# Performance work log

Hardware: AMD Instinct MI355X
Metric: run time of the kernel (lower is better)

Reference implementation:

```python
import jax, jax.numpy as jnp
import numpy as np

N_NODES = 50000
N_EDGES = 600000
IN_DIM = 128
OUT_DIM = 128
NEG_SLOPE = 0.2
LN_EPS = 1e-5


def setup_inputs() -> dict:
    key = jax.random.key(0)
    ks = jax.random.split(key, 8)
    x = jax.random.normal(ks[0], (N_NODES, IN_DIM), dtype=jnp.float32)
    edge_index = jax.random.randint(ks[1], (2, N_EDGES), 0, N_NODES, dtype=jnp.int64)
    glorot = float(np.sqrt(6.0 / (IN_DIM + OUT_DIM)))
    W_l = jax.random.uniform(ks[2], (IN_DIM, OUT_DIM), jnp.float32, -glorot, glorot)
    W_r = jax.random.uniform(ks[3], (IN_DIM, OUT_DIM), jnp.float32, -glorot, glorot)
    att = jax.random.uniform(ks[4], (OUT_DIM,), jnp.float32, -glorot, glorot)
    bias = jnp.zeros((OUT_DIM,), jnp.float32)
    ln_gamma = jnp.ones((OUT_DIM,), jnp.float32)
    ln_beta = jnp.zeros((OUT_DIM,), jnp.float32)
    return {"x": x, "edge_index": edge_index, "W_l": W_l, "W_r": W_r,
            "att": att, "bias": bias, "ln_gamma": ln_gamma, "ln_beta": ln_beta}


def _gatv2_ln(x, edge_index, W_l, W_r, att, bias, ln_gamma, ln_beta):
    N = x.shape[0]
    # add self loops (PyG GATv2Conv default add_self_loops=True)
    loop = jnp.arange(N, dtype=edge_index.dtype)
    src = jnp.concatenate([edge_index[0], loop])  # [E+N]
    dst = jnp.concatenate([edge_index[1], loop])
    x_l = x @ W_l  # [N, D] transformed source features
    x_r = x @ W_r  # [N, D] transformed target features
    # GATv2 edge score: e_ij = a^T LeakyReLU(x_l[src] + x_r[dst])
    h = jax.nn.leaky_relu(x_l[src] + x_r[dst], NEG_SLOPE)  # [E+N, D]
    e = h @ att  # [E+N]
    # segment softmax over incoming edges of each dst node
    m = jax.lax.stop_gradient(jax.ops.segment_max(e, dst, num_segments=N))
    ex = jnp.exp(e - m[dst])
    denom = jax.ops.segment_sum(ex, dst, num_segments=N)
    alpha = ex / denom[dst]  # [E+N] (denom > 0 thanks to self loops)
    # weighted scatter-add aggregation (dropout=0.1 is inference no-op)
    out = jax.ops.segment_sum(alpha[:, None] * x_l[src], dst, num_segments=N)
    out = out + bias  # heads=1, concat=False -> mean over 1 head = identity
    # LayerNorm over feature dim
    mu = jnp.mean(out, axis=-1, keepdims=True)
    var = jnp.var(out, axis=-1, keepdims=True)
    return (out - mu) * jax.lax.rsqrt(var + LN_EPS) * ln_gamma + ln_beta


def reference(x, edge_index, W_l, W_r, att, bias, ln_gamma, ln_beta):
    return _gatv2_ln(x, edge_index, W_l, W_r, att, bias, ln_gamma, ln_beta)
```

## Files before the change

kernel.cpp:

```cpp
#include <hip/hip_runtime.h>
#include <hip/hip_bf16.h>


constexpr int NN  = 50000;
constexpr int NE  = 600000;
constexpr int D   = 128;
constexpr int CAP = 64;
constexpr int MT  = 80;
constexpr int GEMM_THREADS = 320;

typedef __attribute__((ext_vector_type(8))) short bf16x8;
typedef __attribute__((ext_vector_type(4))) float f32x4;

__device__ __forceinline__ ushort f2bf(float f) {
  uint u = __builtin_bit_cast(uint, f);
  return (ushort)((u + 0x7FFFu + ((u >> 16) & 1u)) >> 16);
}
__device__ __forceinline__ float bflo(uint u) { return __builtin_bit_cast(float, u << 16); }
__device__ __forceinline__ float bfhi(uint u) { return __builtin_bit_cast(float, u & 0xFFFF0000u); }
__device__ __forceinline__ void unpack8(uint4 u, float* v) {
  v[0] = bflo(u.x); v[1] = bfhi(u.x);
  v[2] = bflo(u.y); v[3] = bfhi(u.y);
  v[4] = bflo(u.z); v[5] = bfhi(u.z);
  v[6] = bflo(u.w); v[7] = bfhi(u.w);
}

__global__ __launch_bounds__(256) void k_wpack(const float* __restrict__ Wl,
    const float* __restrict__ Wr, ushort* __restrict__ wpk) {
  const int t = blockIdx.x * 256 + threadIdx.x;
  if (t >= 2 * 4 * 8 * 64) return;
  const int lane = t & 63;
  const int ct   = (t >> 6) & 7;
  const int ks   = (t >> 9) & 3;
  const int wh   = t >> 11;
  const float* W = wh ? Wr : Wl;
  const int c  = ct * 16 + (lane & 15);
  const int k0 = ks * 32 + (lane >> 4) * 8;
  ushort v[8];
#pragma unroll
  for (int j = 0; j < 8; ++j) v[j] = f2bf(W[(k0 + j) * D + c]);
  *(bf16x8*)&wpk[(size_t)t * 8] = *(bf16x8*)v;
}

__global__ __launch_bounds__(GEMM_THREADS) void k_gemm(const float* __restrict__ x,
    const ushort* __restrict__ wpk, ushort* __restrict__ xl,
    ushort* __restrict__ xr) {
  __shared__ __align__(16) ushort axs[MT * D];
  const int t = threadIdx.x;
  const int row0 = blockIdx.x * MT;
  for (int ch = t; ch < MT * 16; ch += GEMM_THREADS) {
    const int r = ch >> 4, kc = ch & 15;
    const float4* src = (const float4*)&x[(size_t)(row0 + r) * D + kc * 8];
    const float4 f0 = src[0], f1 = src[1];
    ushort pk[8];
    pk[0] = f2bf(f0.x); pk[1] = f2bf(f0.y); pk[2] = f2bf(f0.z); pk[3] = f2bf(f0.w);
    pk[4] = f2bf(f1.x); pk[5] = f2bf(f1.y); pk[6] = f2bf(f1.z); pk[7] = f2bf(f1.w);
    uint byte = (uint)(r * 256 + kc * 16);
    byte ^= (uint)((r & 7) << 4);
    *(bf16x8*)((char*)axs + byte) = *(bf16x8*)pk;
  }
  __syncthreads();
  const int w = t >> 6, l = t & 63;
  f32x4 accl[8], accr[8];
#pragma unroll
  for (int ct = 0; ct < 8; ++ct) { accl[ct] = (f32x4)0.f; accr[ct] = (f32x4)0.f; }
  const bf16x8* wv = (const bf16x8*)wpk;
  const int rloc = w * 16 + (l & 15);
#pragma unroll
  for (int ks = 0; ks < 4; ++ks) {
    uint byte = (uint)(rloc * 256 + ks * 64 + ((l >> 4) << 4));
    byte ^= (uint)((rloc & 7) << 4);
    const bf16x8 a = *(const bf16x8*)((const char*)axs + byte);
#pragma unroll
    for (int ct = 0; ct < 8; ++ct) {
      const bf16x8 bl = wv[((0 * 4 + ks) * 8 + ct) * 64 + l];
      const bf16x8 br = wv[((1 * 4 + ks) * 8 + ct) * 64 + l];
      accl[ct] = __builtin_amdgcn_mfma_f32_16x16x32_bf16(a, bl, accl[ct], 0, 0, 0);
      accr[ct] = __builtin_amdgcn_mfma_f32_16x16x32_bf16(a, br, accr[ct], 0, 0, 0);
    }
  }
  const int rl0 = w * 16 + ((l >> 4) << 2);
  const int cl  = l & 15;
#pragma unroll
  for (int ct = 0; ct < 8; ++ct) {
    const int col = ct * 16 + cl;
#pragma unroll
    for (int i = 0; i < 4; ++i) {
      const size_t o = (size_t)(row0 + rl0 + i) * D + col;
      xl[o] = f2bf(accl[ct][i]);
      xr[o] = f2bf(accr[ct][i]);
    }
  }
}

__global__ __launch_bounds__(256) void k_fill(const int* __restrict__ ei,
    int* __restrict__ cnt, int* __restrict__ eidx) {
  const int e = blockIdx.x * 256 + threadIdx.x;
  if (e < NE) {
    const int src = ei[e];
    const int dst = ei[NE + e];
    const int pos = atomicAdd(&cnt[dst], 1);
    if (pos < CAP) eidx[dst * CAP + pos] = src;
  }
}

__global__ __launch_bounds__(256) void k_node(const int* __restrict__ cnt,
    const int* __restrict__ eidx,
    const ushort* __restrict__ xl, const ushort* __restrict__ xr,
    const float* __restrict__ att, const float* __restrict__ bias,
    const float* __restrict__ gamma, const float* __restrict__ beta,
    float* __restrict__ out) {
  const int n = blockIdx.x * 4 + (threadIdx.x >> 6);
  const int lane = threadIdx.x & 63;
  const int eg = lane & 3;
  const int ls = lane >> 2;
  const int d0 = ls * 8;
  constexpr float LOG2E = 1.4426950408889634f;

  float vr[8], av[8], vs[8];
  unpack8(*(const uint4*)&xr[(uint)n * D + d0], vr);
  unpack8(*(const uint4*)&xl[(uint)n * D + d0], vs);
  *(float4*)&av[0] = *(const float4*)&att[d0];
  *(float4*)&av[4] = *(const float4*)&att[d0 + 4];

  const int m    = min(cnt[n], CAP);
  const int base = n * CAP;

  float ss = 0.f;
#pragma unroll
  for (int j = 0; j < 8; ++j) {
    float h = vs[j] + vr[j];
    h = fmaxf(h, 0.2f * h);
    ss = fmaf(h, av[j], ss);
  }
  ss += __shfl_xor(ss, 4);
  ss += __shfl_xor(ss, 8);
  ss += __shfl_xor(ss, 16);
  ss += __shfl_xor(ss, 32);
  const float eself = exp2f(ss * LOG2E);

  float acc[8] = {0.f,0.f,0.f,0.f,0.f,0.f,0.f,0.f};
  float den = 0.f;

  int s1 = (eg < m) ? eidx[base + eg] : n;
  uint4 u = *(const uint4*)&xl[(uint)s1 * D + d0];
  s1 = (4 + eg < m) ? eidx[base + 4 + eg] : n;

  for (int p0 = 0; p0 < m; p0 += 4) {
    uint4 un = *(const uint4*)&xl[(uint)s1 * D + d0];
    const int pe2 = p0 + 8 + eg;
    const int s2 = (pe2 < m) ? eidx[base + pe2] : n;
    const bool act = (p0 + eg < m);
    float v[8];
    unpack8(u, v);
    float h0, h1;
    h0 = v[0] + vr[0]; h0 = fmaxf(h0, 0.2f * h0);
    h1 = v[1] + vr[1]; h1 = fmaxf(h1, 0.2f * h1);
    float t0 = fmaf(h0, av[0], h1 * av[1]);
    h0 = v[2] + vr[2]; h0 = fmaxf(h0, 0.2f * h0);
    h1 = v[3] + vr[3]; h1 = fmaxf(h1, 0.2f * h1);
    float t1 = fmaf(h0, av[2], h1 * av[3]);
    h0 = v[4] + vr[4]; h0 = fmaxf(h0, 0.2f * h0);
    h1 = v[5] + vr[5]; h1 = fmaxf(h1, 0.2f * h1);
    float t2 = fmaf(h0, av[4], h1 * av[5]);
    h0 = v[6] + vr[6]; h0 = fmaxf(h0, 0.2f * h0);
    h1 = v[7] + vr[7]; h1 = fmaxf(h1, 0.2f * h1);
    float t3 = fmaf(h0, av[6], h1 * av[7]);
    float s = (t0 + t1) + (t2 + t3);
    s += __shfl_xor(s, 4);
    s += __shfl_xor(s, 8);
    s += __shfl_xor(s, 16);
    s += __shfl_xor(s, 32);
    const float e = act ? exp2f(s * LOG2E) : 0.f;
    den += e;
#pragma unroll
    for (int j = 0; j < 8; ++j) acc[j] = fmaf(e, v[j], acc[j]);
    u = un; s1 = s2;
  }
#pragma unroll
  for (int j = 0; j < 8; ++j) {
    acc[j] += __shfl_xor(acc[j], 1);
    acc[j] += __shfl_xor(acc[j], 2);
  }
  den += __shfl_xor(den, 1);
  den += __shfl_xor(den, 2);
  den += eself;
#pragma unroll
  for (int j = 0; j < 8; ++j) acc[j] = fmaf(eself, vs[j], acc[j]);
  const float inv = 1.0f / den;

  float o[8];
  {
    const float4 b0 = *(const float4*)&bias[d0];
    const float4 b1 = *(const float4*)&bias[d0 + 4];
    o[0] = fmaf(acc[0], inv, b0.x); o[1] = fmaf(acc[1], inv, b0.y);
    o[2] = fmaf(acc[2], inv, b0.z); o[3] = fmaf(acc[3], inv, b0.w);
    o[4] = fmaf(acc[4], inv, b1.x); o[5] = fmaf(acc[5], inv, b1.y);
    o[6] = fmaf(acc[6], inv, b1.z); o[7] = fmaf(acc[7], inv, b1.w);
  }
  float sm = 0.f, sq = 0.f;
#pragma unroll
  for (int j = 0; j < 8; ++j) { sm += o[j]; sq = fmaf(o[j], o[j], sq); }
  sm += __shfl_xor(sm, 4);  sq += __shfl_xor(sq, 4);
  sm += __shfl_xor(sm, 8);  sq += __shfl_xor(sq, 8);
  sm += __shfl_xor(sm, 16); sq += __shfl_xor(sq, 16);
  sm += __shfl_xor(sm, 32); sq += __shfl_xor(sq, 32);
  const float mean = sm * (1.0f / D);
  const float var  = sq * (1.0f / D) - mean * mean;
  const float rstd = rsqrtf(var + 1e-5f);
  if (eg == 0) {
    const float4 g0 = *(const float4*)&gamma[d0];
    const float4 g1 = *(const float4*)&gamma[d0 + 4];
    const float4 be0 = *(const float4*)&beta[d0];
    const float4 be1 = *(const float4*)&beta[d0 + 4];
    float4 o0, o1;
    o0.x = (o[0] - mean) * rstd * g0.x + be0.x;
    o0.y = (o[1] - mean) * rstd * g0.y + be0.y;
    o0.z = (o[2] - mean) * rstd * g0.z + be0.z;
    o0.w = (o[3] - mean) * rstd * g0.w + be0.w;
    o1.x = (o[4] - mean) * rstd * g1.x + be1.x;
    o1.y = (o[5] - mean) * rstd * g1.y + be1.y;
    o1.z = (o[6] - mean) * rstd * g1.z + be1.z;
    o1.w = (o[7] - mean) * rstd * g1.w + be1.w;
    *(float4*)&out[(size_t)n * D + d0]     = o0;
    *(float4*)&out[(size_t)n * D + d0 + 4] = o1;
  }
}

extern "C" void kernel_launch(void* const* d_in, const int* in_sizes, int n_in,
                              void* d_out, int out_size, void* d_ws, size_t ws_size,
                              hipStream_t stream) {
  const float* x     = (const float*)d_in[0];
  const int*   ei    = (const int*)d_in[1];
  const float* Wl    = (const float*)d_in[2];
  const float* Wr    = (const float*)d_in[3];
  const float* att   = (const float*)d_in[4];
  const float* bias  = (const float*)d_in[5];
  const float* gamma = (const float*)d_in[6];
  const float* beta  = (const float*)d_in[7];
  float* out = (float*)d_out;

  char* ws = (char*)d_ws;
  ushort* xl   = (ushort*)ws;
  ushort* xr   = xl + (size_t)NN * D;
  int*    eidx = (int*)(xr + (size_t)NN * D);
  int*    cnt  = eidx + (size_t)NN * CAP;
  ushort* wpk  = (ushort*)(cnt + NN);

  hipMemsetAsync(cnt, 0, NN * sizeof(int), stream);
  k_wpack<<<16, 256, 0, stream>>>(Wl, Wr, wpk);
  k_gemm<<<NN / MT, GEMM_THREADS, 0, stream>>>(x, wpk, xl, xr);
  k_fill<<<(NE + 255) / 256, 256, 0, stream>>>(ei, cnt, eidx);
  k_node<<<NN / 4, 256, 0, stream>>>(cnt, eidx, xl, xr, att, bias, gamma,
                                     beta, out);
}
```

Before: 181.7 us.

## Switch intermediates to fp16 with packed dot2, fuse memset/wpack and gemm/fill kernels

Stores the transformed features xl/xr as fp16 instead of bf16 and uses the fp16 MFMA. In the node kernel the LeakyReLU and attention dot product now run on packed half2 math with fdot2, which cuts ALU work per edge. The count memset is folded into the weight-pack kernel, and the edge-bucketing fill now runs as extra blocks of the GEMM launch, handling four edges per thread with vector loads. This removes two launches and lets the GEMM and fill overlap, at the cost of fp16 range and precision limits on the features and the attention scores.

Result: faster. 167.0 us (-8.1%).

```diff
diff --git a/kernel.cpp b/kernel.cpp
--- a/kernel.cpp
+++ b/kernel.cpp
@@ -1,5 +1,6 @@
 #include <hip/hip_runtime.h>
 #include <hip/hip_bf16.h>
+#include <hip/hip_fp16.h>
 
 
 constexpr int NN  = 50000;
@@ -8,27 +9,27 @@
 constexpr int CAP = 64;
 constexpr int MT  = 80;
 constexpr int GEMM_THREADS = 320;
-
-typedef __attribute__((ext_vector_type(8))) short bf16x8;
+constexpr int GEMM_BLOCKS  = NN / MT;
+constexpr int FILL_BLOCKS  = (NE / 4 + GEMM_THREADS - 1) / GEMM_THREADS;
+
+typedef _Float16 h2    __attribute__((ext_vector_type(2)));
+typedef _Float16 f16x8 __attribute__((ext_vector_type(8)));
 typedef __attribute__((ext_vector_type(4))) float f32x4;
 
-__device__ __forceinline__ ushort f2bf(float f) {
-  uint u = __builtin_bit_cast(uint, f);
-  return (ushort)((u + 0x7FFFu + ((u >> 16) & 1u)) >> 16);
-}
-__device__ __forceinline__ float bflo(uint u) { return __builtin_bit_cast(float, u << 16); }
-__device__ __forceinline__ float bfhi(uint u) { return __builtin_bit_cast(float, u & 0xFFFF0000u); }
-__device__ __forceinline__ void unpack8(uint4 u, float* v) {
-  v[0] = bflo(u.x); v[1] = bfhi(u.x);
-  v[2] = bflo(u.y); v[3] = bfhi(u.y);
-  v[4] = bflo(u.z); v[5] = bfhi(u.z);
-  v[6] = bflo(u.w); v[7] = bfhi(u.w);
-}
-
-__global__ __launch_bounds__(256) void k_wpack(const float* __restrict__ Wl,
-    const float* __restrict__ Wr, ushort* __restrict__ wpk) {
+__device__ __forceinline__ ushort f2h(float f) {
+  const _Float16 h = (_Float16)f;
+  return __builtin_bit_cast(ushort, h);
+}
+
+__global__ __launch_bounds__(256) void k_setup(const float* __restrict__ Wl,
+    const float* __restrict__ Wr, ushort* __restrict__ wpk,
+    int* __restrict__ cnt) {
+  if (blockIdx.x >= 16) {
+    const int i = (blockIdx.x - 16) * 256 + threadIdx.x;
+    if (i < NN) cnt[i] = 0;
+    return;
+  }
   const int t = blockIdx.x * 256 + threadIdx.x;
-  if (t >= 2 * 4 * 8 * 64) return;
   const int lane = t & 63;
   const int ct   = (t >> 6) & 7;
   const int ks   = (t >> 9) & 3;
@@ -38,13 +39,27 @@
   const int k0 = ks * 32 + (lane >> 4) * 8;
   ushort v[8];
 #pragma unroll
-  for (int j = 0; j < 8; ++j) v[j] = f2bf(W[(k0 + j) * D + c]);
-  *(bf16x8*)&wpk[(size_t)t * 8] = *(bf16x8*)v;
-}
-
-__global__ __launch_bounds__(GEMM_THREADS) void k_gemm(const float* __restrict__ x,
+  for (int j = 0; j < 8; ++j) v[j] = f2h(W[(k0 + j) * D + c]);
+  *(f16x8*)&wpk[(size_t)t * 8] = *(const f16x8*)v;
+}
+
+__global__ __launch_bounds__(GEMM_THREADS) void k_mega(const float* __restrict__ x,
     const ushort* __restrict__ wpk, ushort* __restrict__ xl,
-    ushort* __restrict__ xr) {
+    ushort* __restrict__ xr, const int* __restrict__ ei,
+    int* __restrict__ cnt, int* __restrict__ eidx) {
+  if (blockIdx.x >= GEMM_BLOCKS) {
+    const int e0 = ((blockIdx.x - GEMM_BLOCKS) * GEMM_THREADS + threadIdx.x) * 4;
+    if (e0 < NE) {
+      const int4 s4 = *(const int4*)&ei[e0];
+      const int4 d4 = *(const int4*)&ei[NE + e0];
+      int pos;
+      pos = atomicAdd(&cnt[d4.x], 1); if (pos < CAP) eidx[d4.x * CAP + pos] = s4.x;
+      pos = atomicAdd(&cnt[d4.y], 1); if (pos < CAP) eidx[d4.y * CAP + pos] = s4.y;
+      pos = atomicAdd(&cnt[d4.z], 1); if (pos < CAP) eidx[d4.z * CAP + pos] = s4.z;
+      pos = atomicAdd(&cnt[d4.w], 1); if (pos < CAP) eidx[d4.w * CAP + pos] = s4.w;
+    }
+    return;
+  }
   __shared__ __align__(16) ushort axs[MT * D];
   const int t = threadIdx.x;
   const int row0 = blockIdx.x * MT;
@@ -53,30 +68,30 @@
     const float4* src = (const float4*)&x[(size_t)(row0 + r) * D + kc * 8];
     const float4 f0 = src[0], f1 = src[1];
     ushort pk[8];
-    pk[0] = f2bf(f0.x); pk[1] = f2bf(f0.y); pk[2] = f2bf(f0.z); pk[3] = f2bf(f0.w);
-    pk[4] = f2bf(f1.x); pk[5] = f2bf(f1.y); pk[6] = f2bf(f1.z); pk[7] = f2bf(f1.w);
+    pk[0] = f2h(f0.x); pk[1] = f2h(f0.y); pk[2] = f2h(f0.z); pk[3] = f2h(f0.w);
+    pk[4] = f2h(f1.x); pk[5] = f2h(f1.y); pk[6] = f2h(f1.z); pk[7] = f2h(f1.w);
     uint byte = (uint)(r * 256 + kc * 16);
     byte ^= (uint)((r & 7) << 4);
-    *(bf16x8*)((char*)axs + byte) = *(bf16x8*)pk;
+    *(f16x8*)((char*)axs + byte) = *(const f16x8*)pk;
   }
   __syncthreads();
   const int w = t >> 6, l = t & 63;
   f32x4 accl[8], accr[8];
 #pragma unroll
   for (int ct = 0; ct < 8; ++ct) { accl[ct] = (f32x4)0.f; accr[ct] = (f32x4)0.f; }
-  const bf16x8* wv = (const bf16x8*)wpk;
+  const f16x8* wv = (const f16x8*)wpk;
   const int rloc = w * 16 + (l & 15);
 #pragma unroll
   for (int ks = 0; ks < 4; ++ks) {
     uint byte = (uint)(rloc * 256 + ks * 64 + ((l >> 4) << 4));
     byte ^= (uint)((rloc & 7) << 4);
-    const bf16x8 a = *(const bf16x8*)((const char*)axs + byte);
+    const f16x8 a = *(const f16x8*)((const char*)axs + byte);
 #pragma unroll
     for (int ct = 0; ct < 8; ++ct) {
-      const bf16x8 bl = wv[((0 * 4 + ks) * 8 + ct) * 64 + l];
-      const bf16x8 br = wv[((1 * 4 + ks) * 8 + ct) * 64 + l];
-      accl[ct] = __builtin_amdgcn_mfma_f32_16x16x32_bf16(a, bl, accl[ct], 0, 0, 0);
-      accr[ct] = __builtin_amdgcn_mfma_f32_16x16x32_bf16(a, br, accr[ct], 0, 0, 0);
+      const f16x8 bl = wv[((0 * 4 + ks) * 8 + ct) * 64 + l];
+      const f16x8 br = wv[((1 * 4 + ks) * 8 + ct) * 64 + l];
+      accl[ct] = __builtin_amdgcn_mfma_f32_16x16x32_f16(a, bl, accl[ct], 0, 0, 0);
+      accr[ct] = __builtin_amdgcn_mfma_f32_16x16x32_f16(a, br, accr[ct], 0, 0, 0);
     }
   }
   const int rl0 = w * 16 + ((l >> 4) << 2);
@@ -87,20 +102,9 @@
 #pragma unroll
     for (int i = 0; i < 4; ++i) {
       const size_t o = (size_t)(row0 + rl0 + i) * D + col;
-      xl[o] = f2bf(accl[ct][i]);
-      xr[o] = f2bf(accr[ct][i]);
-    }
-  }
-}
-
-__global__ __launch_bounds__(256) void k_fill(const int* __restrict__ ei,
-    int* __restrict__ cnt, int* __restrict__ eidx) {
-  const int e = blockIdx.x * 256 + threadIdx.x;
-  if (e < NE) {
-    const int src = ei[e];
-    const int dst = ei[NE + e];
-    const int pos = atomicAdd(&cnt[dst], 1);
-    if (pos < CAP) eidx[dst * CAP + pos] = src;
+      xl[o] = f2h(accl[ct][i]);
+      xr[o] = f2h(accr[ct][i]);
+    }
   }
 }
 
@@ -116,22 +120,32 @@
   const int ls = lane >> 2;
   const int d0 = ls * 8;
   constexpr float LOG2E = 1.4426950408889634f;
-
-  float vr[8], av[8], vs[8];
-  unpack8(*(const uint4*)&xr[(uint)n * D + d0], vr);
-  unpack8(*(const uint4*)&xl[(uint)n * D + d0], vs);
-  *(float4*)&av[0] = *(const float4*)&att[d0];
-  *(float4*)&av[4] = *(const float4*)&att[d0 + 4];
+  const h2 c02 = {(_Float16)0.2f, (_Float16)0.2f};
+
+  const f16x8 vrh = __builtin_bit_cast(f16x8, *(const uint4*)&xr[(uint)n * D + d0]);
+  const f16x8 vsh = __builtin_bit_cast(f16x8, *(const uint4*)&xl[(uint)n * D + d0]);
+  h2 av2[4];
+  {
+    const float4 a0 = *(const float4*)&att[d0];
+    const float4 a1 = *(const float4*)&att[d0 + 4];
+    av2[0] = h2{(_Float16)a0.x, (_Float16)a0.y};
+    av2[1] = h2{(_Float16)a0.z, (_Float16)a0.w};
+    av2[2] = h2{(_Float16)a1.x, (_Float16)a1.y};
+    av2[3] = h2{(_Float16)a1.z, (_Float16)a1.w};
+  }
+  h2 vr2[4];
+#pragma unroll
+  for (int q = 0; q < 4; ++q) vr2[q] = h2{vrh[2*q], vrh[2*q+1]};
 
   const int m    = min(cnt[n], CAP);
   const int base = n * CAP;
 
   float ss = 0.f;
 #pragma unroll
-  for (int j = 0; j < 8; ++j) {
-    float h = vs[j] + vr[j];
-    h = fmaxf(h, 0.2f * h);
-    ss = fmaf(h, av[j], ss);
+  for (int q = 0; q < 4; ++q) {
+    h2 h = h2{vsh[2*q], vsh[2*q+1]} + vr2[q];
+    h = __builtin_elementwise_max(h, h * c02);
+    ss = __builtin_amdgcn_fdot2(h, av2[q], ss, false);
   }
   ss += __shfl_xor(ss, 4);
   ss += __shfl_xor(ss, 8);
@@ -147,26 +161,18 @@
   s1 = (4 + eg < m) ? eidx[base + 4 + eg] : n;
 
   for (int p0 = 0; p0 < m; p0 += 4) {
-    uint4 un = *(const uint4*)&xl[(uint)s1 * D + d0];
+    const uint4 un = *(const uint4*)&xl[(uint)s1 * D + d0];
     const int pe2 = p0 + 8 + eg;
     const int s2 = (pe2 < m) ? eidx[base + pe2] : n;
     const bool act = (p0 + eg < m);
-    float v[8];
-    unpack8(u, v);
-    float h0, h1;
-    h0 = v[0] + vr[0]; h0 = fmaxf(h0, 0.2f * h0);
-    h1 = v[1] + vr[1]; h1 = fmaxf(h1, 0.2f * h1);
-    float t0 = fmaf(h0, av[0], h1 * av[1]);
-    h0 = v[2] + vr[2]; h0 = fmaxf(h0, 0.2f * h0);
-    h1 = v[3] + vr[3]; h1 = fmaxf(h1, 0.2f * h1);
-    float t1 = fmaf(h0, av[2], h1 * av[3]);
-    h0 = v[4] + vr[4]; h0 = fmaxf(h0, 0.2f * h0);
-    h1 = v[5] + vr[5]; h1 = fmaxf(h1, 0.2f * h1);
-    float t2 = fmaf(h0, av[4], h1 * av[5]);
-    h0 = v[6] + vr[6]; h0 = fmaxf(h0, 0.2f * h0);
-    h1 = v[7] + vr[7]; h1 = fmaxf(h1, 0.2f * h1);
-    float t3 = fmaf(h0, av[6], h1 * av[7]);
-    float s = (t0 + t1) + (t2 + t3);
+    const f16x8 vh = __builtin_bit_cast(f16x8, u);
+    float s = 0.f;
+#pragma unroll
+    for (int q = 0; q < 4; ++q) {
+      h2 h = h2{vh[2*q], vh[2*q+1]} + vr2[q];
+      h = __builtin_elementwise_max(h, h * c02);
+      s = __builtin_amdgcn_fdot2(h, av2[q], s, false);
+    }
     s += __shfl_xor(s, 4);
     s += __shfl_xor(s, 8);
     s += __shfl_xor(s, 16);
@@ -174,7 +180,7 @@
     const float e = act ? exp2f(s * LOG2E) : 0.f;
     den += e;
 #pragma unroll
-    for (int j = 0; j < 8; ++j) acc[j] = fmaf(e, v[j], acc[j]);
+    for (int j = 0; j < 8; ++j) acc[j] = fmaf(e, (float)vh[j], acc[j]);
     u = un; s1 = s2;
   }
 #pragma unroll
@@ -186,7 +192,7 @@
   den += __shfl_xor(den, 2);
   den += eself;
 #pragma unroll
-  for (int j = 0; j < 8; ++j) acc[j] = fmaf(eself, vs[j], acc[j]);
+  for (int j = 0; j < 8; ++j) acc[j] = fmaf(eself, (float)vsh[j], acc[j]);
   const float inv = 1.0f / den;
 
   float o[8];
@@ -247,10 +253,9 @@
   int*    cnt  = eidx + (size_t)NN * CAP;
   ushort* wpk  = (ushort*)(cnt + NN);
 
-  hipMemsetAsync(cnt, 0, NN * sizeof(int), stream);
-  k_wpack<<<16, 256, 0, stream>>>(Wl, Wr, wpk);
-  k_gemm<<<NN / MT, GEMM_THREADS, 0, stream>>>(x, wpk, xl, xr);
-  k_fill<<<(NE + 255) / 256, 256, 0, stream>>>(ei, cnt, eidx);
+  k_setup<<<16 + (NN + 255) / 256, 256, 0, stream>>>(Wl, Wr, wpk, cnt);
+  k_mega<<<GEMM_BLOCKS + FILL_BLOCKS, GEMM_THREADS, 0, stream>>>(
+      x, wpk, xl, xr, ei, cnt, eidx);
   k_node<<<NN / 4, 256, 0, stream>>>(cnt, eidx, xl, xr, att, bias, gamma,
                                      beta, out);
 }
```
